# Kernel tuning notes

Hardware: AMD Instinct MI355X
Metric: run time of the kernel (lower is better)

Reference implementation:

```python
import jax, jax.numpy as jnp
import numpy as np

B, T, C, HS = 4, 4096, 1024, 64  # batch, seq, n_embd, head_size


def setup_inputs() -> dict:
    key = jax.random.key(0)
    kx, kq, kk, kv = jax.random.split(key, 4)
    s = 1.0 / np.sqrt(C)  # Linear-like init scale
    return {
        "x": jax.random.normal(kx, (B, T, C), dtype=jnp.float32),
        "Wq": jax.random.normal(kq, (C, HS), dtype=jnp.float32) * s,
        "bq": jnp.zeros((HS,), dtype=jnp.float32),
        "Wk": jax.random.normal(kk, (C, HS), dtype=jnp.float32) * s,
        "bk": jnp.zeros((HS,), dtype=jnp.float32),
        "Wv": jax.random.normal(kv, (C, HS), dtype=jnp.float32) * s,
        "bv": jnp.zeros((HS,), dtype=jnp.float32),
    }


def reference(x, Wq, bq, Wk, bk, Wv, bv):
    # x: [B,T,C]
    q = x @ Wq + bq          # [B,T,HS]
    k = x @ Wk + bk          # [B,T,HS]
    v = x @ Wv + bv          # [B,T,HS]
    att = jnp.einsum("bqh,bkh->bqk", q, k)  # [B,T,T]
    att = att * (C ** -0.5)  # NOTE: scales by n_embd, not head_size (faithful to source)
    causal = jnp.tril(jnp.ones((T, T), dtype=bool))
    att = jnp.where(causal, att, -jnp.inf)
    att = jax.nn.softmax(att, axis=-1)
    # dropout p=0.0 (eval): identity
    out = jnp.einsum("bqk,bkh->bqh", att, v)  # [B,T,HS]
    return out
```

## Files before the change

kernel.cpp:

```cpp
#include <hip/hip_runtime.h>
#include <hip/hip_bf16.h>
#include <math.h>

#define B 4
#define T 4096
#define C 1024
#define HS 64

typedef __attribute__((ext_vector_type(8))) short short8;
typedef __attribute__((ext_vector_type(4))) float f32x4;
typedef __attribute__((ext_vector_type(16))) float f32x16;

#define MFMA16(a, b, c) __builtin_amdgcn_mfma_f32_16x16x32_bf16((a), (b), (c), 0, 0, 0)
#define MFMA32(a, b, c) __builtin_amdgcn_mfma_f32_32x32x16_bf16((a), (b), (c), 0, 0, 0)

#define QSCALE 0.0450842200278f

static __device__ __forceinline__ unsigned short f2bf(float f) {
  union { float f; unsigned u; } v; v.f = f;
  unsigned r = v.u + 0x7FFFu + ((v.u >> 16) & 1u);
  return (unsigned short)(r >> 16);
}

static __device__ __forceinline__ unsigned pack_bf2(float lo, float hi2) {
  union { __hip_bfloat16 h; unsigned short u; } a, c;
  a.h = __float2bfloat16(lo); c.h = __float2bfloat16(hi2);
  return (unsigned)a.u | ((unsigned)c.u << 16);
}

__global__ __launch_bounds__(256) void conv_w_kernel(
    const float* __restrict__ Wq, const float* __restrict__ Wk,
    const float* __restrict__ Wv, unsigned short* __restrict__ Wtf) {
  const int wi = blockIdx.x >> 4;
  const int c0 = (blockIdx.x & 15) * 64;
  const float* W = (wi == 0) ? Wq : (wi == 1) ? Wk : Wv;
  __shared__ float ws[64][65];
  const int t = threadIdx.x;
  const int r = t >> 2;
  const int cb = (t & 3) * 16;
#pragma unroll
  for (int j = 0; j < 4; ++j) {
    const f32x4 v = *(const f32x4*)&W[(size_t)(c0 + r) * HS + cb + 4 * j];
    ws[cb + 4 * j + 0][r] = v[0];
    ws[cb + 4 * j + 1][r] = v[1];
    ws[cb + 4 * j + 2][r] = v[2];
    ws[cb + 4 * j + 3][r] = v[3];
  }
  __syncthreads();
  const int h  = t >> 2;
  const int rb = (t & 3) * 16;
  const int n   = wi * 64 + h;
  const int nt  = n >> 4;
  const int col = n & 15;
#pragma unroll
  for (int j = 0; j < 2; ++j) {
    const int cbase = c0 + rb + j * 8;
    union { short8 s8; unsigned short u[8]; } o;
#pragma unroll
    for (int e = 0; e < 8; ++e) o.u[e] = f2bf(ws[h][rb + j * 8 + e]);
    const int kc128 = cbase >> 7;
    const int k32   = (cbase >> 5) & 3;
    const int grp   = (cbase >> 3) & 3;
    const size_t idx =
        ((size_t)(kc128 * 48 + k32 * 12 + nt) * 512 + (grp * 16 + col) * 8);
    *(short8*)(Wtf + idx) = o.s8;
  }
}

__global__ __launch_bounds__(512, 2) void proj_kernel(
    const float* __restrict__ x, const unsigned short* __restrict__ Wtf,
    const float* __restrict__ bq, const float* __restrict__ bk,
    const float* __restrict__ bv,
    unsigned short* __restrict__ Qf, unsigned short* __restrict__ Kf,
    unsigned short* __restrict__ Vf) {
  const int m0   = blockIdx.x * 64;
  const int w    = threadIdx.x >> 6;
  const int lane = threadIdx.x & 63;
  const int col  = lane & 15, grp = lane >> 4;
  const int wm   = w >> 2;
  const int wn   = w & 3;
  const int phase = blockIdx.x & 7;

  __shared__ unsigned short A_lds[2][64 * 128];
  __shared__ unsigned short B_lds[2][48][512];

  const int arow  = threadIdx.x >> 3;
  const int akoff = (threadIdx.x & 7) * 16;
  const float* xp = x + (size_t)(m0 + arow) * C + akoff;

  f32x4 acc[2][3];
#pragma unroll
  for (int mf = 0; mf < 2; ++mf)
#pragma unroll
    for (int jj = 0; jj < 3; ++jj) acc[mf][jj] = (f32x4){0.f, 0.f, 0.f, 0.f};

  auto kcOf = [&](int it) { return ((it + phase) & 7) * 128; };

  auto stageB = [&](int nb, int kc) {
    const int kc128 = kc >> 7;
#pragma unroll
    for (int j = 0; j < 6; ++j) {
      const int f = w * 6 + j;
      const unsigned short* src =
          Wtf + ((size_t)(kc128 * 48 + f) * 512) + lane * 8;
      __builtin_amdgcn_global_load_lds(
          (const __attribute__((address_space(1))) void*)src,
          (__attribute__((address_space(3))) void*)&B_lds[nb][f][0],
          16, 0, 0);
    }
  };

  auto loadAreg = [&](int kc, f32x4 (&r)[4]) {
#pragma unroll
    for (int i = 0; i < 4; ++i) r[i] = *(const f32x4*)(xp + kc + 4 * i);
  };

  auto writeA = [&](int nb, const f32x4 (&r)[4]) {
    union { short8 s8[2]; unsigned short u[16]; } o;
#pragma unroll
    for (int i = 0; i < 4; ++i)
#pragma unroll
      for (int e = 0; e < 4; ++e) o.u[4 * i + e] = f2bf(r[i][e]);
    const int b0 = arow * 256 + (threadIdx.x & 7) * 32;
    const int s  = (arow & 7) << 4;
    char* base = (char*)&A_lds[nb][0];
    *(short8*)(base + ((b0     ) ^ s)) = o.s8[0];
    *(short8*)(base + ((b0 + 16) ^ s)) = o.s8[1];
  };

  auto readA = [&](int buf, int mf, int k32) {
    const int row = wm * 32 + mf * 16 + col;
    const int b = row * 256 + ((k32 * 64 + grp * 16) ^ ((col & 7) << 4));
    return *(const short8*)((const char*)&A_lds[buf][0] + b);
  };

  auto compute = [&](int buf) {
#pragma unroll
    for (int k32 = 0; k32 < 4; ++k32) {
      const short8 a0 = readA(buf, 0, k32);
      const short8 a1 = readA(buf, 1, k32);
#pragma unroll
      for (int jj = 0; jj < 3; ++jj) {
        const short8 bf =
            *(const short8*)&B_lds[buf][k32 * 12 + wn * 3 + jj][(size_t)lane * 8];
        acc[0][jj] = MFMA16(a0, bf, acc[0][jj]);
        acc[1][jj] = MFMA16(a1, bf, acc[1][jj]);
      }
    }
  };

  f32x4 arA[4];
  loadAreg(kcOf(0), arA);
  stageB(0, kcOf(0));
  writeA(0, arA);
  loadAreg(kcOf(1), arA);
  __syncthreads();

  for (int it = 0; it < 8; ++it) {
    const int buf = it & 1;
    if (it < 7) stageB(buf ^ 1, kcOf(it + 1));
    compute(buf);
    if (it < 7) {
      writeA(buf ^ 1, arA);
      if (it < 6) loadAreg(kcOf(it + 2), arA);
    }
    __syncthreads();
  }

  unsigned short (*E)[12][512] =
      (unsigned short (*)[12][512]) & A_lds[0][0];

#pragma unroll
  for (int mf = 0; mf < 2; ++mf) {
#pragma unroll
    for (int jj = 0; jj < 3; ++jj) {
      const int n = wn * 48 + jj * 16 + col;
      const float bias = (n < 64) ? bq[n] : (n < 128) ? bk[n - 64] : bv[n - 128];
#pragma unroll
      for (int r = 0; r < 4; ++r) {
        const int rloc = mf * 16 + 4 * grp + r;
        const float v = acc[mf][jj][r] + bias;
        if (n < 64) {
          E[wm][n >> 4][(((n >> 3) & 1) * 32 + rloc) * 8 + (n & 7)] =
              f2bf(v * QSCALE);
        } else if (n < 128) {
          const int d = n - 64;
          E[wm][4 + (d >> 4)][(((d >> 3) & 1) * 32 + rloc) * 8 + (d & 7)] =
              f2bf(v);
        } else {
          const int d = n - 128;
          const int vi = ((d >> 5) << 1) + ((rloc >> 4) & 1);
          E[wm][8 + vi][(((rloc >> 3) & 1) * 32 + (d & 31)) * 8 + (rloc & 7)] =
              f2bf(v);
        }
      }
    }
  }
  __syncthreads();

  {
    const int bb    = m0 >> 12;
    const int blkg0 = (m0 & (T - 1)) >> 5;
#pragma unroll
    for (int j = 0; j < 3; ++j) {
      const int fidx  = w * 3 + j;
      const int blk_l = fidx / 12;
      const int ft    = fidx % 12;
      const short8 val = *(const short8*)&E[blk_l][ft][lane * 8];
      const size_t fb = ((size_t)(bb * 128 + blkg0 + blk_l) * 4);
      unsigned short* dst;
      if (ft < 4)      dst = Qf + (fb + ft) * 512;
      else if (ft < 8) dst = Kf + (fb + (ft - 4)) * 512;
      else             dst = Vf + (fb + (ft - 8)) * 512;
      *(short8*)(dst + lane * 8) = val;
    }
  }
}

__global__ __launch_bounds__(512, 2) void attn_kernel(
    const unsigned short* __restrict__ Qf,
    const unsigned short* __restrict__ Kf,
    const unsigned short* __restrict__ Vf,
    float* __restrict__ out) {
  const int x8 = blockIdx.x & 7;
  const int b  = x8 >> 1;
  const int p  = ((blockIdx.x >> 3) << 1) | (x8 & 1);

  const int w8   = threadIdx.x >> 6;
  const int g    = w8 >> 2;
  const int w    = w8 & 3;
  const int lane = threadIdx.x & 63;
  const int q    = lane & 31;
  const int hi   = lane >> 5;
  const int qt   = g ? (127 - p) : p;
  const int qbase = qt * 32;
  const int qg    = qbase + q;

  __shared__ float accL[8][64][33];
  __shared__ float lL[8][32], invL[2][32];

  const unsigned short* Qp = Qf + ((size_t)(b * 128 + qt) * 4) * 512;
  const unsigned short* Kb = Kf + ((size_t)b * 128) * 4 * 512;
  const unsigned short* Vb = Vf + ((size_t)b * 128) * 4 * 512;

  short8 qf[4];
#pragma unroll
  for (int j = 0; j < 4; ++j)
    qf[j] = *(const short8*)(Qp + j * 512 + lane * 8);

  f32x16 acc0, acc1;
#pragma unroll
  for (int r = 0; r < 16; ++r) { acc0[r] = 0.f; acc1[r] = 0.f; }
  float lsum = 0.f;

  const int nkv = qt + 1;

  short8 kA[4], vA[4], kB[4], vB[4];

  auto loadKV = [&](int kb, short8 (&kd)[4], short8 (&vd)[4]) {
    const unsigned short* pk = Kb + (size_t)kb * 2048 + lane * 8;
    kd[0] = *(const short8*)(pk);
    kd[1] = *(const short8*)(pk + 512);
    kd[2] = *(const short8*)(pk + 1024);
    kd[3] = *(const short8*)(pk + 1536);
    const unsigned short* pv = Vb + (size_t)kb * 2048 + lane * 8;
    vd[0] = *(const short8*)(pv);
    vd[1] = *(const short8*)(pv + 512);
    vd[2] = *(const short8*)(pv + 1024);
    vd[3] = *(const short8*)(pv + 1536);
  };

  auto step = [&](int kb, short8 (&kc)[4], short8 (&vc)[4],
                  short8 (&kn)[4], short8 (&vn)[4]) {
    int knb = kb + 4;
    if (knb > 127) knb = 127;
    loadKV(knb, kn, vn);

    f32x16 s;
#pragma unroll
    for (int r = 0; r < 16; ++r) s[r] = -8.0f;
    s = MFMA32(kc[0], qf[0], s);
    s = MFMA32(kc[1], qf[1], s);
    s = MFMA32(kc[2], qf[2], s);
    s = MFMA32(kc[3], qf[3], s);

    float pe[16];
    if (kb == qt) {
      const int qrel = qg - kb * 32;
#pragma unroll
      for (int r = 0; r < 16; ++r) {
        const int key = (r & 3) + 8 * (r >> 2) + 4 * hi;
        const float v = exp2f(s[r]);
        pe[r] = (key <= qrel) ? v : 0.f;
      }
    } else {
#pragma unroll
      for (int r = 0; r < 16; ++r) pe[r] = exp2f(s[r]);
    }
#pragma unroll
    for (int r = 0; r < 16; ++r) lsum += pe[r];

    unsigned own[8];
#pragma unroll
    for (int j = 0; j < 8; ++j) own[j] = pack_bf2(pe[2 * j], pe[2 * j + 1]);
    unsigned a0v = own[0], b0v = own[2];
    unsigned a1v = own[1], b1v = own[3];
    unsigned a2v = own[4], b2v = own[6];
    unsigned a3v = own[5], b3v = own[7];
    asm("v_permlane32_swap_b32 %0, %1" : "+v"(a0v), "+v"(b0v));
    asm("v_permlane32_swap_b32 %0, %1" : "+v"(a1v), "+v"(b1v));
    asm("v_permlane32_swap_b32 %0, %1" : "+v"(a2v), "+v"(b2v));
    asm("v_permlane32_swap_b32 %0, %1" : "+v"(a3v), "+v"(b3v));
    union U { short8 s8; unsigned u[4]; };
    U p0, p1;
    p0.u[0] = a0v; p0.u[1] = a1v; p0.u[2] = b0v; p0.u[3] = b1v;
    p1.u[0] = a2v; p1.u[1] = a3v; p1.u[2] = b2v; p1.u[3] = b3v;

    acc0 = MFMA32(vc[0], p0.s8, acc0);
    acc0 = MFMA32(vc[1], p1.s8, acc0);
    acc1 = MFMA32(vc[2], p0.s8, acc1);
    acc1 = MFMA32(vc[3], p1.s8, acc1);
  };

  if (w < nkv) {
    loadKV(w, kA, vA);
    int kb = w;
    while (true) {
      step(kb, kA, vA, kB, vB); kb += 4; if (kb >= nkv) break;
      step(kb, kB, vB, kA, vA); kb += 4; if (kb >= nkv) break;
    }
  }

  lsum += __shfl_xor(lsum, 32, 64);
  if (hi == 0) lL[w8][q] = lsum;
#pragma unroll
  for (int r = 0; r < 16; ++r) {
    const int d = (r & 3) + 8 * (r >> 2) + 4 * hi;
    accL[w8][d][q]      = acc0[r];
    accL[w8][d + 32][q] = acc1[r];
  }
  __syncthreads();
  if (threadIdx.x < 64) {
    const int g2 = threadIdx.x >> 5;
    const int qq = threadIdx.x & 31;
    const float L = lL[g2 * 4 + 0][qq] + lL[g2 * 4 + 1][qq] +
                    lL[g2 * 4 + 2][qq] + lL[g2 * 4 + 3][qq];
    invL[g2][qq] = 1.f / L;
  }
  __syncthreads();
  {
    const int tid2 = threadIdx.x & 255;
#pragma unroll
    for (int pp = 0; pp < 8; ++pp) {
      const int qq = (tid2 >> 6) + 4 * pp;
      const int d  = tid2 & 63;
      const float v = accL[g * 4 + 0][d][qq] + accL[g * 4 + 1][d][qq] +
                      accL[g * 4 + 2][d][qq] + accL[g * 4 + 3][d][qq];
      out[(size_t)(b * T + qbase + qq) * HS + d] = v * invL[g][qq];
    }
  }
}

extern "C" void kernel_launch(void* const* d_in, const int* in_sizes, int n_in,
                              void* d_out, int out_size, void* d_ws, size_t ws_size,
                              hipStream_t stream) {
  const float* x  = (const float*)d_in[0];
  const float* Wq = (const float*)d_in[1];
  const float* bq = (const float*)d_in[2];
  const float* Wk = (const float*)d_in[3];
  const float* bk = (const float*)d_in[4];
  const float* Wv = (const float*)d_in[5];
  const float* bv = (const float*)d_in[6];
  float* out = (float*)d_out;

  unsigned short* Qf  = (unsigned short*)d_ws;
  unsigned short* Kf  = Qf + (size_t)B * T * HS;
  unsigned short* Vf  = Kf + (size_t)B * T * HS;
  unsigned short* Wtf = Vf + (size_t)B * T * HS;

  conv_w_kernel<<<48, 256, 0, stream>>>(Wq, Wk, Wv, Wtf);
  proj_kernel<<<B * T / 64, 512, 0, stream>>>(x, Wtf, bq, bk, bv, Qf, Kf, Vf);
  attn_kernel<<<B * 64, 512, 0, stream>>>(Qf, Kf, Vf, out);
}
```

Measured before the change: 49.54 us.

## Software-pipeline QK and PV MFMAs across key blocks to overlap softmax

Restructures the per-wave key loop so the QK^T MFMAs for the next block are issued before the PV MFMAs of the previous block, with the exp/pack/permlane work placed in between. This is meant to hide the dependency stall between score computation, exponentiation and the PV matmul by giving the matrix unit independent work. The KV prefetch is also moved after the compute. In exchange it keeps more fragments live, which raises register pressure and could reduce occupancy.

```diff
diff --git a/kernel.cpp b/kernel.cpp
--- a/kernel.cpp
+++ b/kernel.cpp
@@ -256,6 +256,7 @@
   const int nkv = qt + 1;
 
   short8 kA[4], vA[4], kB[4], vB[4];
+  short8 pp0, pp1;
 
   auto loadKV = [&](int kb, short8 (&kd)[4], short8 (&vd)[4]) {
     const unsigned short* pk = Kb + (size_t)kb * 2048 + lane * 8;
@@ -270,12 +271,7 @@
     vd[3] = *(const short8*)(pv + 1536);
   };
 
-  auto step = [&](int kb, short8 (&kc)[4], short8 (&vc)[4],
-                  short8 (&kn)[4], short8 (&vn)[4]) {
-    int knb = kb + 4;
-    if (knb > 127) knb = 127;
-    loadKV(knb, kn, vn);
-
+  auto computeS = [&](short8 (&kc)[4]) {
     f32x16 s;
 #pragma unroll
     for (int r = 0; r < 16; ++r) s[r] = -8.0f;
@@ -283,7 +279,17 @@
     s = MFMA32(kc[1], qf[1], s);
     s = MFMA32(kc[2], qf[2], s);
     s = MFMA32(kc[3], qf[3], s);
-
+    return s;
+  };
+
+  auto doPV = [&](short8 (&vc)[4]) {
+    acc0 = MFMA32(vc[0], pp0, acc0);
+    acc0 = MFMA32(vc[1], pp1, acc0);
+    acc1 = MFMA32(vc[2], pp0, acc1);
+    acc1 = MFMA32(vc[3], pp1, acc1);
+  };
+
+  auto doPE = [&](int kb, const f32x16& s) {
     float pe[16];
     if (kb == qt) {
       const int qrel = qg - kb * 32;
@@ -312,22 +318,43 @@
     asm("v_permlane32_swap_b32 %0, %1" : "+v"(a2v), "+v"(b2v));
     asm("v_permlane32_swap_b32 %0, %1" : "+v"(a3v), "+v"(b3v));
     union U { short8 s8; unsigned u[4]; };
-    U p0, p1;
-    p0.u[0] = a0v; p0.u[1] = a1v; p0.u[2] = b0v; p0.u[3] = b1v;
-    p1.u[0] = a2v; p1.u[1] = a3v; p1.u[2] = b2v; p1.u[3] = b3v;
-
-    acc0 = MFMA32(vc[0], p0.s8, acc0);
-    acc0 = MFMA32(vc[1], p1.s8, acc0);
-    acc1 = MFMA32(vc[2], p0.s8, acc1);
-    acc1 = MFMA32(vc[3], p1.s8, acc1);
+    U r0, r1;
+    r0.u[0] = a0v; r0.u[1] = a1v; r0.u[2] = b0v; r0.u[3] = b1v;
+    r1.u[0] = a2v; r1.u[1] = a3v; r1.u[2] = b2v; r1.u[3] = b3v;
+    pp0 = r0.s8; pp1 = r1.s8;
   };
 
   if (w < nkv) {
-    loadKV(w, kA, vA);
     int kb = w;
+    loadKV(kb, kA, vA);
+    {
+      int knb = kb + 4; if (knb > 127) knb = 127;
+      loadKV(knb, kB, vB);
+    }
+    {
+      const f32x16 s = computeS(kA);
+      doPE(kb, s);
+    }
+    kb += 4;
     while (true) {
-      step(kb, kA, vA, kB, vB); kb += 4; if (kb >= nkv) break;
-      step(kb, kB, vB, kA, vA); kb += 4; if (kb >= nkv) break;
+      if (kb >= nkv) { doPV(vA); break; }
+      {
+        const f32x16 s = computeS(kB);
+        doPV(vA);
+        doPE(kb, s);
+        int knb = kb + 4; if (knb > 127) knb = 127;
+        loadKV(knb, kA, vA);
+        kb += 4;
+      }
+      if (kb >= nkv) { doPV(vB); break; }
+      {
+        const f32x16 s = computeS(kA);
+        doPV(vB);
+        doPE(kb, s);
+        int knb = kb + 4; if (knb > 127) knb = 127;
+        loadKV(knb, kB, vB);
+        kb += 4;
+      }
     }
   }
 
```

New measurement: 64.75 us. 30.7% more time.

## Load projection operands directly into registers instead of staging through LDS

Applied to the files above, without the earlier changes.

The QKV projection kernel no longer stages x and the pre-packed weights through double-buffered shared memory. Each wave now loads its own MFMA fragments straight from global memory into registers, with a two-deep register double buffer over 64-wide K chunks. This removes the LDS writes, the swizzled reads and the per-iteration barriers. In exchange, x rows and weight fragments are read redundantly by several waves through the cache, global access coalescing changes, and register pressure rises.

```diff
diff --git a/kernel.cpp b/kernel.cpp
--- a/kernel.cpp
+++ b/kernel.cpp
@@ -79,14 +79,9 @@
   const int col  = lane & 15, grp = lane >> 4;
   const int wm   = w >> 2;
   const int wn   = w & 3;
-  const int phase = blockIdx.x & 7;
-
-  __shared__ unsigned short A_lds[2][64 * 128];
-  __shared__ unsigned short B_lds[2][48][512];
-
-  const int arow  = threadIdx.x >> 3;
-  const int akoff = (threadIdx.x & 7) * 16;
-  const float* xp = x + (size_t)(m0 + arow) * C + akoff;
+  const int phase = blockIdx.x & 15;
+
+  __shared__ unsigned short E_lds[2][12][512];
 
   f32x4 acc[2][3];
 #pragma unroll
@@ -94,81 +89,70 @@
 #pragma unroll
     for (int jj = 0; jj < 3; ++jj) acc[mf][jj] = (f32x4){0.f, 0.f, 0.f, 0.f};
 
-  auto kcOf = [&](int it) { return ((it + phase) & 7) * 128; };
-
-  auto stageB = [&](int nb, int kc) {
+  auto kcOf = [&](int it) { return ((it + phase) & 15) * 64; };
+
+  auto loadA = [&](int kc, f32x4 (&af)[8]) {
+#pragma unroll
+    for (int mf = 0; mf < 2; ++mf)
+#pragma unroll
+      for (int k32 = 0; k32 < 2; ++k32) {
+        const float* p = x + (size_t)(m0 + wm * 32 + mf * 16 + col) * C +
+                         kc + k32 * 32 + grp * 8;
+        af[(mf * 2 + k32) * 2 + 0] = *(const f32x4*)p;
+        af[(mf * 2 + k32) * 2 + 1] = *(const f32x4*)(p + 4);
+      }
+  };
+  auto loadB = [&](int kc, short8 (&bf)[6]) {
     const int kc128 = kc >> 7;
-#pragma unroll
-    for (int j = 0; j < 6; ++j) {
-      const int f = w * 6 + j;
-      const unsigned short* src =
-          Wtf + ((size_t)(kc128 * 48 + f) * 512) + lane * 8;
-      __builtin_amdgcn_global_load_lds(
-          (const __attribute__((address_space(1))) void*)src,
-          (__attribute__((address_space(3))) void*)&B_lds[nb][f][0],
-          16, 0, 0);
-    }
-  };
-
-  auto loadAreg = [&](int kc, f32x4 (&r)[4]) {
-#pragma unroll
-    for (int i = 0; i < 4; ++i) r[i] = *(const f32x4*)(xp + kc + 4 * i);
-  };
-
-  auto writeA = [&](int nb, const f32x4 (&r)[4]) {
-    union { short8 s8[2]; unsigned short u[16]; } o;
-#pragma unroll
-    for (int i = 0; i < 4; ++i)
-#pragma unroll
-      for (int e = 0; e < 4; ++e) o.u[4 * i + e] = f2bf(r[i][e]);
-    const int b0 = arow * 256 + (threadIdx.x & 7) * 32;
-    const int s  = (arow & 7) << 4;
-    char* base = (char*)&A_lds[nb][0];
-    *(short8*)(base + ((b0     ) ^ s)) = o.s8[0];
-    *(short8*)(base + ((b0 + 16) ^ s)) = o.s8[1];
-  };
-
-  auto readA = [&](int buf, int mf, int k32) {
-    const int row = wm * 32 + mf * 16 + col;
-    const int b = row * 256 + ((k32 * 64 + grp * 16) ^ ((col & 7) << 4));
-    return *(const short8*)((const char*)&A_lds[buf][0] + b);
-  };
-
-  auto compute = [&](int buf) {
-#pragma unroll
-    for (int k32 = 0; k32 < 4; ++k32) {
-      const short8 a0 = readA(buf, 0, k32);
-      const short8 a1 = readA(buf, 1, k32);
-#pragma unroll
-      for (int jj = 0; jj < 3; ++jj) {
-        const short8 bf =
-            *(const short8*)&B_lds[buf][k32 * 12 + wn * 3 + jj][(size_t)lane * 8];
-        acc[0][jj] = MFMA16(a0, bf, acc[0][jj]);
-        acc[1][jj] = MFMA16(a1, bf, acc[1][jj]);
+    const int k32b  = (kc >> 5) & 3;
+#pragma unroll
+    for (int k32 = 0; k32 < 2; ++k32)
+#pragma unroll
+      for (int jj = 0; jj < 3; ++jj)
+        bf[k32 * 3 + jj] = *(const short8*)(
+            Wtf + ((size_t)(kc128 * 48 + (k32b + k32) * 12 + wn * 3 + jj) * 512)
+                + lane * 8);
+  };
+  auto cvtA = [&](const f32x4 (&af)[8], short8 (&a)[4]) {
+#pragma unroll
+    for (int i = 0; i < 4; ++i) {
+      short8 t;
+#pragma unroll
+      for (int e = 0; e < 4; ++e) {
+        t[e]     = (short)f2bf(af[2 * i][e]);
+        t[4 + e] = (short)f2bf(af[2 * i + 1][e]);
       }
-    }
-  };
-
-  f32x4 arA[4];
-  loadAreg(kcOf(0), arA);
-  stageB(0, kcOf(0));
-  writeA(0, arA);
-  loadAreg(kcOf(1), arA);
-  __syncthreads();
-
-  for (int it = 0; it < 8; ++it) {
-    const int buf = it & 1;
-    if (it < 7) stageB(buf ^ 1, kcOf(it + 1));
-    compute(buf);
-    if (it < 7) {
-      writeA(buf ^ 1, arA);
-      if (it < 6) loadAreg(kcOf(it + 2), arA);
-    }
-    __syncthreads();
-  }
-
-  unsigned short (*E)[12][512] =
-      (unsigned short (*)[12][512]) & A_lds[0][0];
+      a[i] = t;
+    }
+  };
+  auto compute = [&](const short8 (&a)[4], const short8 (&bf)[6]) {
+#pragma unroll
+    for (int mf = 0; mf < 2; ++mf)
+#pragma unroll
+      for (int k32 = 0; k32 < 2; ++k32)
+#pragma unroll
+        for (int jj = 0; jj < 3; ++jj)
+          acc[mf][jj] = MFMA16(a[mf * 2 + k32], bf[k32 * 3 + jj], acc[mf][jj]);
+  };
+
+  f32x4 afA[8], afB[8];
+  short8 bfA[6], bfB[6];
+  short8 a[4];
+
+  loadA(kcOf(0), afA);
+  loadB(kcOf(0), bfA);
+  for (int it = 0; it < 16; it += 2) {
+    loadA(kcOf(it + 1), afB);
+    loadB(kcOf(it + 1), bfB);
+    cvtA(afA, a);
+    compute(a, bfA);
+    if (it + 2 < 16) {
+      loadA(kcOf(it + 2), afA);
+      loadB(kcOf(it + 2), bfA);
+    }
+    cvtA(afB, a);
+    compute(a, bfB);
+  }
 
 #pragma unroll
   for (int mf = 0; mf < 2; ++mf) {
@@ -181,16 +165,16 @@
         const int rloc = mf * 16 + 4 * grp + r;
         const float v = acc[mf][jj][r] + bias;
         if (n < 64) {
-          E[wm][n >> 4][(((n >> 3) & 1) * 32 + rloc) * 8 + (n & 7)] =
+          E_lds[wm][n >> 4][(((n >> 3) & 1) * 32 + rloc) * 8 + (n & 7)] =
               f2bf(v * QSCALE);
         } else if (n < 128) {
           const int d = n - 64;
-          E[wm][4 + (d >> 4)][(((d >> 3) & 1) * 32 + rloc) * 8 + (d & 7)] =
+          E_lds[wm][4 + (d >> 4)][(((d >> 3) & 1) * 32 + rloc) * 8 + (d & 7)] =
               f2bf(v);
         } else {
           const int d = n - 128;
           const int vi = ((d >> 5) << 1) + ((rloc >> 4) & 1);
-          E[wm][8 + vi][(((rloc >> 3) & 1) * 32 + (d & 31)) * 8 + (rloc & 7)] =
+          E_lds[wm][8 + vi][(((rloc >> 3) & 1) * 32 + (d & 31)) * 8 + (rloc & 7)] =
               f2bf(v);
         }
       }
@@ -206,7 +190,7 @@
       const int fidx  = w * 3 + j;
       const int blk_l = fidx / 12;
       const int ft    = fidx % 12;
-      const short8 val = *(const short8*)&E[blk_l][ft][lane * 8];
+      const short8 val = *(const short8*)&E_lds[blk_l][ft][lane * 8];
       const size_t fb = ((size_t)(bb * 128 + blkg0 + blk_l) * 4);
       unsigned short* dst;
       if (ft < 4)      dst = Qf + (fb + ft) * 512;
```

Measured after the change: 69.47 us. 40.2% more time.
